# Performance work log

Hardware: AMD Instinct MI355X
Metric: run time of the kernel (lower is better)

The kernel has to match this reference:

```python
import jax, jax.numpy as jnp
import numpy as np

K = 9      # kernel size
DIL = 2    # dilation
PAD = 8    # padding -> same-size output


def unfold(x):
    """nd2col: (B,C,H,W) -> (B,C,K,K,H,W) patches with dilation/padding."""
    B, C, H, W = x.shape
    xp = jnp.pad(x, ((0, 0), (0, 0), (PAD, PAD), (PAD, PAD)))
    cols = jnp.stack(
        [xp[:, :, i * DIL:i * DIL + H, j * DIL:j * DIL + W]
         for i in range(K) for j in range(K)], axis=2)
    return cols.reshape(B, C, K, K, H, W)


def pac_kernel(f):
    """Gaussian adaptive kernel: exp(-0.5*||f_nbr - f_center||^2), shape (B,1,K,K,H,W)."""
    # center of the dilated patch (K//2, K//2) is the pixel itself
    d = unfold(f) - f[:, :, None, None, :, :]
    return jnp.exp(-0.5 * jnp.sum(d * d, axis=1, keepdims=True))


def pacconv(x, k, w, b):
    """Pixel-adaptive conv: unfold, modulate by guidance kernel, contract with weight."""
    cols = unfold(x)                                  # (B,Cin,K,K,H,W)
    out = jnp.einsum('bcklhw,ockl->bohw', cols * k, w)
    return out + b[None, :, None, None]


def setup_inputs() -> dict:
    key = jax.random.key(0)
    ks = jax.random.split(key, 6)
    B, C, H, W = 1, 32, 128, 128
    x = jax.random.normal(ks[0], (B, C, H, W), jnp.float32)
    f = jax.random.normal(ks[1], (B, C, H, W), jnp.float32)
    fan_in = C * K * K
    bound = float(1.0 / np.sqrt(fan_in))
    W1 = jax.random.uniform(ks[2], (32, C, K, K), jnp.float32, -bound, bound)
    b1 = jax.random.uniform(ks[3], (32,), jnp.float32, -bound, bound)
    W2 = jax.random.uniform(ks[4], (32, 32, K, K), jnp.float32, -bound, bound)
    b2 = jax.random.uniform(ks[5], (32,), jnp.float32, -bound, bound)
    return {"x": x, "f": f, "W1": W1, "b1": b1, "W2": W2, "b2": b2}


def reference(x, f, W1, b1, W2, b2):
    k = pac_kernel(f)  # same guidance for both layers -> identical kernel
    h = pacconv(x, k, W1, b1)
    return pacconv(h, k, W2, b2)
```

## Files before the change

### kernel.cpp

```cpp
#include <hip/hip_runtime.h>

#define HH 128
#define WW 128
#define NPIX 16384
#define NC 32
#define NO 32
#define KS 9
#define TAPS 81
#define DIL 2
#define PAD 8
#define SMAX 27.6310211159f
#define NW (NO * NC * TAPS)
#define CAP 262144

#define BUILD_MASK(P, M0, M1) do {                                          \
        M0 = 0ull; M1 = 0u;                                                 \
        _Pragma("unroll")                                                   \
        for (int i_ = 0; i_ < 7; ++i_) {                                    \
            unsigned v_ = mask2[i_ * NPIX + (P)];                           \
            unsigned m_ = (v_ & 31u) | (((v_ >> 8) & 15u) << 5);            \
            M0 |= (unsigned long long)m_ << (9 * i_);                       \
        }                                                                   \
        {                                                                   \
            unsigned v7_ = mask2[7 * NPIX + (P)];                           \
            unsigned v8_ = mask2[8 * NPIX + (P)];                           \
            unsigned m7_ = (v7_ & 31u) | (((v7_ >> 8) & 15u) << 5);         \
            unsigned m8_ = (v8_ & 31u) | (((v8_ >> 8) & 15u) << 5);         \
            M0 |= (unsigned long long)(m7_ & 1u) << 63;                     \
            M1 = (m7_ >> 1) | (m8_ << 8);                                   \
        }                                                                   \
    } while (0)

__global__ __launch_bounds__(256) void front2_kernel(
    const float* __restrict__ x, const float* __restrict__ f,
    const float* __restrict__ W1, const float* __restrict__ W2,
    const float* __restrict__ b1,
    float* __restrict__ hd, float* __restrict__ kbuf,
    unsigned short* __restrict__ mask2, float* __restrict__ Mm,
    float* __restrict__ W1t, float* __restrict__ W2t,
    float* __restrict__ outz)
{
    const int bid = blockIdx.x;
    const int tid = threadIdx.x;
    __shared__ float shbuf[2048];

    if (bid < 1152) {
        const int pixblk = bid & 63, iz = bid >> 6;
        const int i = iz >> 1, z = iz & 1;
        const int pix = pixblk * 256 + tid;
        const int hh = pix >> 7, ww = pix & (WW - 1);
        float fc[NC];
#pragma unroll
        for (int c = 0; c < NC; ++c) fc[c] = f[c * NPIX + pix];
        const int qh = hh + i * DIL - PAD;
        const bool vh = (unsigned)qh < HH;
        const int j0 = z * 5;
        unsigned pmask = 0;
#pragma unroll
        for (int jj = 0; jj < 5; ++jj) {
            int j = j0 + jj;
            if (j < KS) {
                int qw = ww + j * DIL - PAD;
                bool valid = vh & ((unsigned)qw < WW);
                int q = valid ? (qh * WW + qw) : pix;
                float s0 = 0.f, s1 = 0.f, s2 = 0.f, s3 = 0.f;
#pragma unroll
                for (int c4 = 0; c4 < 8; ++c4) {
                    float d0 = f[(4 * c4 + 0) * NPIX + q] - fc[4 * c4 + 0];
                    float d1 = f[(4 * c4 + 1) * NPIX + q] - fc[4 * c4 + 1];
                    float d2 = f[(4 * c4 + 2) * NPIX + q] - fc[4 * c4 + 2];
                    float d3 = f[(4 * c4 + 3) * NPIX + q] - fc[4 * c4 + 3];
                    s0 = fmaf(d0, d0, s0); s1 = fmaf(d1, d1, s1);
                    s2 = fmaf(d2, d2, s2); s3 = fmaf(d3, d3, s3);
                }
                float s = (s0 + s1) + (s2 + s3);
                bool live = valid && (s <= SMAX) && !(i == 4 && j == 4);
                if (live) {
                    pmask |= 1u << jj;
                    kbuf[(i * KS + j) * NPIX + pix] = __expf(-0.5f * s);
                }
            }
        }
        ((unsigned char*)mask2)[2 * (i * NPIX + pix) + z] = (unsigned char)pmask;
        return;
    }

    if (bid < 1664) {
        const int r = bid - 1152;
        const int o0 = (r >> 6) * 4;
        const int pix = (r & 63) * 256 + tid;
        if (tid < 128)
            shbuf[tid] = W1[((o0 + (tid >> 5)) * NC + (tid & 31)) * TAPS + 40];
        __syncthreads();
        float x0[NC];
#pragma unroll
        for (int c = 0; c < NC; ++c) x0[c] = x[c * NPIX + pix];
        float a0 = 0.f, a1 = 0.f, a2 = 0.f, a3 = 0.f;
#pragma unroll
        for (int c = 0; c < NC; ++c) {
            float xv = x0[c];
            a0 = fmaf(xv, shbuf[0 * NC + c], a0);
            a1 = fmaf(xv, shbuf[1 * NC + c], a1);
            a2 = fmaf(xv, shbuf[2 * NC + c], a2);
            a3 = fmaf(xv, shbuf[3 * NC + c], a3);
        }
        hd[(o0 + 0) * NPIX + pix] = a0 + b1[o0 + 0];
        hd[(o0 + 1) * NPIX + pix] = a1 + b1[o0 + 1];
        hd[(o0 + 2) * NPIX + pix] = a2 + b1[o0 + 2];
        hd[(o0 + 3) * NPIX + pix] = a3 + b1[o0 + 3];
        return;
    }

    if (bid < 1792) {
        float4 z4 = make_float4(0.f, 0.f, 0.f, 0.f);
        for (int t = (bid - 1664) * 256 + tid; t < (NO * NPIX) / 4;
             t += 128 * 256)
            ((float4*)outz)[t] = z4;
        return;
    }

    if (bid < 1873) {
        const int T = bid - 1792;
        float* w2c_l = shbuf;
        float* w1t_l = shbuf + 1024;
        for (int t = tid; t < 1024; t += 256) {
            w2c_l[t] = W2[t * TAPS + 40];
            w1t_l[t] = W1[t * TAPS + T];
        }
        __syncthreads();
        for (int idx = tid; idx < 1024; idx += 256) {
            int o = idx >> 5, cp = idx & 31;
            float acc = 0.f;
#pragma unroll
            for (int c = 0; c < NC; ++c)
                acc = fmaf(w2c_l[o * NC + c], w1t_l[c * NC + cp], acc);
            Mm[(T * NO + o) * NC + cp] = acc;
        }
        return;
    }

    for (int t = (bid - 1873) * 256 + tid; t < NW; t += 64 * 256) {
        int o = t / (NC * TAPS);
        int r = t - o * (NC * TAPS);
        int c = r / TAPS;
        int tap = r - c * TAPS;
        int d = (tap * NO + o) * NC + c;
        W1t[d] = W1[t];
        W2t[d] = W2[t];
    }
}

__global__ __launch_bounds__(256) void back2_kernel(
    const float* __restrict__ x, const float* __restrict__ hd,
    const float* __restrict__ kbuf, const unsigned short* __restrict__ mask2,
    const float* __restrict__ Mm, const float* __restrict__ W1t,
    const float* __restrict__ W2t, const float* __restrict__ W2,
    const float* __restrict__ b2, float* __restrict__ out)
{
    const int bid = blockIdx.x;
    const int tid = threadIdx.x;

    if (bid < 512) {
        __shared__ float wsm[4 * NC];
        const int o0 = (bid >> 6) * 4;
        const int pix = (bid & 63) * 256 + tid;
        if (tid < 128)
            wsm[tid] = W2[((o0 + (tid >> 5)) * NC + (tid & 31)) * TAPS + 40];
        __syncthreads();
        float h0[NC];
#pragma unroll
        for (int c = 0; c < NC; ++c) h0[c] = hd[c * NPIX + pix];
        float a0 = 0.f, a1 = 0.f, a2 = 0.f, a3 = 0.f;
#pragma unroll
        for (int c = 0; c < NC; ++c) {
            float hv = h0[c];
            a0 = fmaf(hv, wsm[0 * NC + c], a0);
            a1 = fmaf(hv, wsm[1 * NC + c], a1);
            a2 = fmaf(hv, wsm[2 * NC + c], a2);
            a3 = fmaf(hv, wsm[3 * NC + c], a3);
        }
        atomicAdd(&out[(o0 + 0) * NPIX + pix], a0 + b2[o0 + 0]);
        atomicAdd(&out[(o0 + 1) * NPIX + pix], a1 + b2[o0 + 1]);
        atomicAdd(&out[(o0 + 2) * NPIX + pix], a2 + b2[o0 + 2]);
        atomicAdd(&out[(o0 + 3) * NPIX + pix], a3 + b2[o0 + 3]);
        return;
    }

    __shared__ float u_lds[8][NC];
    const int hw = tid >> 5;
    const int lane = tid & 31;
    const int pbase = (bid - 512) * 32;

    for (int pp = hw; pp < 32; pp += 8) {
        const int p = pbase + pp;
        unsigned long long A0; unsigned A1;
        BUILD_MASK(p, A0, A1);
        while (A0 || A1) {
            int T;
            if (A0) { T = __builtin_ctzll(A0); A0 &= A0 - 1; }
            else    { T = 64 + __builtin_ctz(A1); A1 &= A1 - 1; }
            const int ii = T / KS, jj = T - KS * ii;
            const int q = p + (ii * DIL - PAD) * WW + (jj * DIL - PAD);
            const float kv = kbuf[T * NPIX + p];

            float w2r[NC], mr[NC];
            {
                const float4* w2p = (const float4*)(W2t + (T * NO + lane) * NC);
                const float4* mp  = (const float4*)(Mm  + (T * NO + lane) * NC);
#pragma unroll
                for (int c4 = 0; c4 < 8; ++c4) {
                    float4 w4 = w2p[c4], m4 = mp[c4];
                    w2r[4 * c4 + 0] = w4.x; w2r[4 * c4 + 1] = w4.y;
                    w2r[4 * c4 + 2] = w4.z; w2r[4 * c4 + 3] = w4.w;
                    mr[4 * c4 + 0] = m4.x; mr[4 * c4 + 1] = m4.y;
                    mr[4 * c4 + 2] = m4.z; mr[4 * c4 + 3] = m4.w;
                }
            }

            float dot = 0.f;
#pragma unroll
            for (int c = 0; c < NC; ++c) {
                dot = fmaf(w2r[c], hd[c * NPIX + q], dot);
                dot = fmaf(mr[c],  x[c * NPIX + q],  dot);
            }

            float dsum = 0.f;
            unsigned long long B0; unsigned B1;
            BUILD_MASK(q, B0, B1);
            while (B0 || B1) {
                int T2;
                if (B0) { T2 = __builtin_ctzll(B0); B0 &= B0 - 1; }
                else    { T2 = 64 + __builtin_ctz(B1); B1 &= B1 - 1; }
                const int i2 = T2 / KS, j2 = T2 - KS * i2;
                const int q2 = q + (i2 * DIL - PAD) * WW + (j2 * DIL - PAD);
                const float kv2 = kbuf[T2 * NPIX + q];
                const float4* w1p =
                    (const float4*)(W1t + (T2 * NO + lane) * NC);
                float u = 0.f;
#pragma unroll
                for (int c4 = 0; c4 < 8; ++c4) {
                    float4 w4 = w1p[c4];
                    u = fmaf(w4.x, x[(4 * c4 + 0) * NPIX + q2], u);
                    u = fmaf(w4.y, x[(4 * c4 + 1) * NPIX + q2], u);
                    u = fmaf(w4.z, x[(4 * c4 + 2) * NPIX + q2], u);
                    u = fmaf(w4.w, x[(4 * c4 + 3) * NPIX + q2], u);
                }
                u_lds[hw][lane] = u;
                float dd = 0.f;
#pragma unroll
                for (int c = 0; c < NC; ++c)
                    dd = fmaf(w2r[c], u_lds[hw][c], dd);
                dsum = fmaf(kv2, dd, dsum);
            }
            atomicAdd(&out[lane * NPIX + p], kv * (dot + dsum));
        }
    }
}

__global__ __launch_bounds__(64) void zero_cnt_kernel(unsigned* __restrict__ cnt)
{
    if (threadIdx.x == 0) *cnt = 0u;
}

__device__ __forceinline__ void sparse_body(
    const float* __restrict__ in, const float* __restrict__ Wt,
    const unsigned* __restrict__ cnt, const uint2* __restrict__ list,
    float* __restrict__ out, unsigned gid, unsigned stride)
{
    unsigned n = *cnt;
    if (n > CAP) n = CAP;
    const unsigned total = n * 32u;
    for (unsigned it = gid; it < total; it += stride) {
        unsigned e = it >> 5;
        int o = (int)(it & 31u);
        uint2 me = list[e];
        int pix = (int)(me.x & 16383u);
        int T = (int)(me.x >> 14);
        float kv = __uint_as_float(me.y);
        int ii = T / KS, jj = T - KS * ii;
        int q = pix + (ii * DIL - PAD) * WW + (jj * DIL - PAD);
        const float4* __restrict__ wp =
            (const float4*)(Wt + (T * NO + o) * NC);
        float t0 = 0.f, t1 = 0.f, t2 = 0.f, t3 = 0.f;
#pragma unroll
        for (int c4 = 0; c4 < 8; ++c4) {
            float4 w4 = wp[c4];
            t0 = fmaf(in[(4 * c4 + 0) * NPIX + q], w4.x, t0);
            t1 = fmaf(in[(4 * c4 + 1) * NPIX + q], w4.y, t1);
            t2 = fmaf(in[(4 * c4 + 2) * NPIX + q], w4.z, t2);
            t3 = fmaf(in[(4 * c4 + 3) * NPIX + q], w4.w, t3);
        }
        atomicAdd(&out[o * NPIX + pix], kv * ((t0 + t1) + (t2 + t3)));
    }
}

__global__ __launch_bounds__(256) void front_kernel(
    const float* __restrict__ x, const float* __restrict__ f,
    const float* __restrict__ W1, const float* __restrict__ W2,
    const float* __restrict__ b1,
    float* __restrict__ h, unsigned* __restrict__ cnt,
    uint2* __restrict__ list, float* __restrict__ W1t,
    float* __restrict__ W2t, float* __restrict__ outz)
{
    const int y = blockIdx.y;
    const int tid = threadIdx.x;

    if (y < 41) {
        const int pix = blockIdx.x * 256 + tid;
        const int hh = pix >> 7, ww = pix & (WW - 1);
        float fc[NC];
#pragma unroll
        for (int c = 0; c < NC; ++c) fc[c] = f[c * NPIX + pix];
#pragma unroll
        for (int u = 0; u < 2; ++u) {
            int T = 2 * y + u;
            if (T >= TAPS || T == 40) continue;
            int ii = T / KS, jj = T - KS * ii;
            int qh = hh + ii * DIL - PAD;
            int qw = ww + jj * DIL - PAD;
            bool valid = ((unsigned)qh < HH) & ((unsigned)qw < WW);
            int q = valid ? (qh * WW + qw) : pix;
            float s0 = 0.f, s1 = 0.f, s2 = 0.f, s3 = 0.f;
#pragma unroll
            for (int c4 = 0; c4 < 8; ++c4) {
                float d0 = f[(4 * c4 + 0) * NPIX + q] - fc[4 * c4 + 0];
                float d1 = f[(4 * c4 + 1) * NPIX + q] - fc[4 * c4 + 1];
                float d2 = f[(4 * c4 + 2) * NPIX + q] - fc[4 * c4 + 2];
                float d3 = f[(4 * c4 + 3) * NPIX + q] - fc[4 * c4 + 3];
                s0 = fmaf(d0, d0, s0); s1 = fmaf(d1, d1, s1);
                s2 = fmaf(d2, d2, s2); s3 = fmaf(d3, d3, s3);
            }
            float s = (s0 + s1) + (s2 + s3);
            if (valid && (s <= SMAX)) {
                unsigned idx = atomicAdd(cnt, 1u);
                if (idx < CAP)
                    list[idx] = make_uint2(
                        (unsigned)pix | ((unsigned)T << 14),
                        __float_as_uint(__expf(-0.5f * s)));
            }
        }
        return;
    }

    if (y < 49) {
        const int o0 = (y - 41) * 4;
        __shared__ float wsm[4 * NC];
        if (tid < 128) {
            int o = tid >> 5, c = tid & 31;
            wsm[tid] = W1[((o0 + o) * NC + c) * TAPS + 40];
        }
        __syncthreads();
        const int pix = blockIdx.x * 256 + tid;
        float x0[NC];
#pragma unroll
        for (int c = 0; c < NC; ++c) x0[c] = x[c * NPIX + pix];
        float a0 = 0.f, a1 = 0.f, a2 = 0.f, a3 = 0.f;
#pragma unroll
        for (int c = 0; c < NC; ++c) {
            float xv = x0[c];
            a0 = fmaf(xv, wsm[0 * NC + c], a0);
            a1 = fmaf(xv, wsm[1 * NC + c], a1);
            a2 = fmaf(xv, wsm[2 * NC + c], a2);
            a3 = fmaf(xv, wsm[3 * NC + c], a3);
        }
        h[(o0 + 0) * NPIX + pix] = a0 + b1[o0 + 0];
        h[(o0 + 1) * NPIX + pix] = a1 + b1[o0 + 1];
        h[(o0 + 2) * NPIX + pix] = a2 + b1[o0 + 2];
        h[(o0 + 3) * NPIX + pix] = a3 + b1[o0 + 3];
        return;
    }

    if (y == 49) {
        float4 z = make_float4(0.f, 0.f, 0.f, 0.f);
        for (int t = blockIdx.x * 256 + tid; t < (NO * NPIX) / 4; t += 64 * 256)
            ((float4*)outz)[t] = z;
        return;
    }

    for (int t = blockIdx.x * 256 + tid; t < NW; t += 64 * 256) {
        int o = t / (NC * TAPS);
        int r = t - o * (NC * TAPS);
        int c = r / TAPS;
        int tap = r - c * TAPS;
        int d = (tap * NO + o) * NC + c;
        W1t[d] = W1[t];
        W2t[d] = W2[t];
    }
}

__global__ __launch_bounds__(256) void sparse1_kernel(
    const float* __restrict__ x, const float* __restrict__ W1t,
    const unsigned* __restrict__ cnt, const uint2* __restrict__ list,
    float* __restrict__ h)
{
    sparse_body(x, W1t, cnt, list, h,
                blockIdx.x * 256 + threadIdx.x, gridDim.x * 256);
}

__global__ __launch_bounds__(256) void back_kernel(
    const float* __restrict__ h, const float* __restrict__ W2,
    const float* __restrict__ W2t, const float* __restrict__ b2,
    const unsigned* __restrict__ cnt, const uint2* __restrict__ list,
    float* __restrict__ out)
{
    const int y = blockIdx.y;
    const int tid = threadIdx.x;
    if (y < 8) {
        const int o0 = y * 4;
        __shared__ float wsm[4 * NC];
        if (tid < 128) {
            int o = tid >> 5, c = tid & 31;
            wsm[tid] = W2[((o0 + o) * NC + c) * TAPS + 40];
        }
        __syncthreads();
        const int pix = blockIdx.x * 256 + tid;
        float h0[NC];
#pragma unroll
        for (int c = 0; c < NC; ++c) h0[c] = h[c * NPIX + pix];
        float a0 = 0.f, a1 = 0.f, a2 = 0.f, a3 = 0.f;
#pragma unroll
        for (int c = 0; c < NC; ++c) {
            float hv = h0[c];
            a0 = fmaf(hv, wsm[0 * NC + c], a0);
            a1 = fmaf(hv, wsm[1 * NC + c], a1);
            a2 = fmaf(hv, wsm[2 * NC + c], a2);
            a3 = fmaf(hv, wsm[3 * NC + c], a3);
        }
        atomicAdd(&out[(o0 + 0) * NPIX + pix], a0 + b2[o0 + 0]);
        atomicAdd(&out[(o0 + 1) * NPIX + pix], a1 + b2[o0 + 1]);
        atomicAdd(&out[(o0 + 2) * NPIX + pix], a2 + b2[o0 + 2]);
        atomicAdd(&out[(o0 + 3) * NPIX + pix], a3 + b2[o0 + 3]);
        return;
    }
    sparse_body(h, W2t, cnt, list, out,
                blockIdx.x * 256 + tid, 64 * 256);
}

#define CHUNK 27
#define NCHUNK 3
#define KMIN 1e-6f
__global__ __launch_bounds__(256) void pac_layer_fuse(
    const float* __restrict__ in, const float* __restrict__ f,
    const float* __restrict__ Wt, const float* __restrict__ bias,
    float* __restrict__ out)
{
    __shared__ float wl[NC * CHUNK * 8];
    const int og = blockIdx.y;
    const int pix = blockIdx.x * 256 + threadIdx.x;
    const int h = pix >> 7, w = pix & (WW - 1);
    float acc[8];
#pragma unroll
    for (int i = 0; i < 8; ++i) acc[i] = 0.f;
    float fc[NC];
#pragma unroll
    for (int c = 0; c < NC; ++c) fc[c] = f[c * NPIX + pix];
    for (int ch = 0; ch < NCHUNK; ++ch) {
        __syncthreads();
        for (int idx = threadIdx.x; idx < NC * CHUNK * 8; idx += 256) {
            int t = idx % CHUNK;
            int c = (idx / CHUNK) % NC;
            int o = idx / (CHUNK * NC);
            wl[(c * CHUNK + t) * 8 + o] =
                Wt[(og * 8 + o) * (NC * TAPS) + c * TAPS + ch * CHUNK + t];
        }
        __syncthreads();
        for (int t = 0; t < CHUNK; ++t) {
            int tap = ch * CHUNK + t;
            int qh = h + (tap / KS) * DIL - PAD;
            int qw = w + (tap % KS) * DIL - PAD;
            bool valid = ((unsigned)qh < HH) & ((unsigned)qw < WW);
            int q = qh * WW + qw;
            float s = 0.f;
#pragma unroll
            for (int c = 0; c < NC; ++c) {
                float fn = valid ? f[c * NPIX + q] : 0.f;
                float d = fn - fc[c];
                s = fmaf(d, d, s);
            }
            float kv = __expf(-0.5f * s);
            if (__all((kv < KMIN) | (!valid))) continue;
            const float* wpp = &wl[t * 8];
#pragma unroll 8
            for (int c = 0; c < NC; ++c) {
                float v = valid ? in[c * NPIX + q] : 0.f;
                v *= kv;
#pragma unroll
                for (int o = 0; o < 8; ++o)
                    acc[o] = fmaf(v, wpp[c * CHUNK * 8 + o], acc[o]);
            }
        }
    }
#pragma unroll
    for (int o = 0; o < 8; ++o)
        out[(og * 8 + o) * NPIX + pix] = acc[o] + bias[og * 8 + o];
}

extern "C" void kernel_launch(void* const* d_in, const int* in_sizes, int n_in,
                              void* d_out, int out_size, void* d_ws, size_t ws_size,
                              hipStream_t stream)
{
    (void)in_sizes; (void)n_in; (void)out_size;
    const float* x  = (const float*)d_in[0];
    const float* f  = (const float*)d_in[1];
    const float* W1 = (const float*)d_in[2];
    const float* b1 = (const float*)d_in[3];
    const float* W2 = (const float*)d_in[4];
    const float* b2 = (const float*)d_in[5];
    float* out = (float*)d_out;

    float* ws = (float*)d_ws;
    float* hd   = ws;
    float* kbuf = hd + NO * NPIX;
    float* W1t  = kbuf + TAPS * NPIX;
    float* W2t  = W1t + NW;
    float* Mm   = W2t + NW;
    unsigned short* mask2 = (unsigned short*)(Mm + TAPS * NO * NC);
    const size_t need_main =
        (size_t)(NO * NPIX + TAPS * NPIX + 2 * NW + TAPS * NO * NC) * 4
        + (size_t)KS * NPIX * 2;
    float* hA   = ws;
    float* W1tA = ws + NO * NPIX;
    float* W2tA = W1tA + NW;
    unsigned* cnt = (unsigned*)(W2tA + NW);
    uint2* list = (uint2*)(cnt + 16);
    const size_t need_fb =
        (size_t)(NO * NPIX + 2 * NW + 16) * 4 + (size_t)CAP * 8;

    if (ws_size >= need_main) {
        front2_kernel<<<dim3(1937), 256, 0, stream>>>(
            x, f, W1, W2, b1, hd, kbuf, mask2, Mm, W1t, W2t, out);
        back2_kernel<<<dim3(1024), 256, 0, stream>>>(
            x, hd, kbuf, mask2, Mm, W1t, W2t, W2, b2, out);
    } else if (ws_size >= need_fb) {
        zero_cnt_kernel<<<dim3(1), 64, 0, stream>>>(cnt);
        front_kernel<<<dim3(64, 51), 256, 0, stream>>>(
            x, f, W1, W2, b1, hA, cnt, list, W1tA, W2tA, out);
        sparse1_kernel<<<dim3(128), 256, 0, stream>>>(x, W1tA, cnt, list, hA);
        back_kernel<<<dim3(64, 9), 256, 0, stream>>>(
            hA, W2, W2tA, b2, cnt, list, out);
    } else {
        float* hbuf = ws;
        pac_layer_fuse<<<dim3(64, 4), 256, 0, stream>>>(x, f, W1, b1, hbuf);
        pac_layer_fuse<<<dim3(64, 4), 256, 0, stream>>>(hbuf, f, W2, b2, out);
    }
}
```

Measured before the change: 120.3 us.

## Store tap masks per pixel contiguously and give each back-kernel warp one pixel

The front kernel now splits each kernel row into three groups of three taps instead of two groups of five. It writes the per-pixel mask bytes contiguously, 32 bytes per pixel. The back kernel builds the 81-bit tap mask with two 16-byte vector loads instead of nine strided short loads. Each half-warp group now handles a single pixel and the back grid grows from 1024 to 2560 blocks, which spreads the irregular sparse work across more blocks. The trade-offs are more front blocks, a larger mask buffer and more launch overhead.

```diff
diff --git a/kernel.cpp b/kernel.cpp
--- a/kernel.cpp
+++ b/kernel.cpp
@@ -13,22 +13,26 @@
 #define NW (NO * NC * TAPS)
 #define CAP 262144
 
-#define BUILD_MASK(P, M0, M1) do {                                          \
+#define BUILD_MASK32(P, M0, M1) do {                                        \
+        const uint4* mp_ = (const uint4*)(mask32 + (size_t)(P) * 32);       \
+        uint4 ma_ = mp_[0], mb_ = mp_[1];                                   \
+        unsigned w_[8] = { ma_.x, ma_.y, ma_.z, ma_.w,                      \
+                           mb_.x, mb_.y, mb_.z, mb_.w };                    \
         M0 = 0ull; M1 = 0u;                                                 \
+        unsigned m9_[9];                                                    \
         _Pragma("unroll")                                                   \
-        for (int i_ = 0; i_ < 7; ++i_) {                                    \
-            unsigned v_ = mask2[i_ * NPIX + (P)];                           \
-            unsigned m_ = (v_ & 31u) | (((v_ >> 8) & 15u) << 5);            \
-            M0 |= (unsigned long long)m_ << (9 * i_);                       \
+        for (int i_ = 0; i_ < 9; ++i_) {                                    \
+            int k0_ = 3 * i_, k1_ = 3 * i_ + 1, k2_ = 3 * i_ + 2;           \
+            unsigned b0_ = (w_[k0_ >> 2] >> ((k0_ & 3) * 8)) & 7u;          \
+            unsigned b1_ = (w_[k1_ >> 2] >> ((k1_ & 3) * 8)) & 7u;          \
+            unsigned b2_ = (w_[k2_ >> 2] >> ((k2_ & 3) * 8)) & 7u;          \
+            m9_[i_] = b0_ | (b1_ << 3) | (b2_ << 6);                        \
         }                                                                   \
-        {                                                                   \
-            unsigned v7_ = mask2[7 * NPIX + (P)];                           \
-            unsigned v8_ = mask2[8 * NPIX + (P)];                           \
-            unsigned m7_ = (v7_ & 31u) | (((v7_ >> 8) & 15u) << 5);         \
-            unsigned m8_ = (v8_ & 31u) | (((v8_ >> 8) & 15u) << 5);         \
-            M0 |= (unsigned long long)(m7_ & 1u) << 63;                     \
-            M1 = (m7_ >> 1) | (m8_ << 8);                                   \
-        }                                                                   \
+        _Pragma("unroll")                                                   \
+        for (int i_ = 0; i_ < 7; ++i_)                                      \
+            M0 |= (unsigned long long)m9_[i_] << (9 * i_);                  \
+        M0 |= (unsigned long long)(m9_[7] & 1u) << 63;                      \
+        M1 = (m9_[7] >> 1) | (m9_[8] << 8);                                 \
     } while (0)
 
 __global__ __launch_bounds__(256) void front2_kernel(
@@ -36,7 +40,7 @@
     const float* __restrict__ W1, const float* __restrict__ W2,
     const float* __restrict__ b1,
     float* __restrict__ hd, float* __restrict__ kbuf,
-    unsigned short* __restrict__ mask2, float* __restrict__ Mm,
+    unsigned char* __restrict__ mask32, float* __restrict__ Mm,
     float* __restrict__ W1t, float* __restrict__ W2t,
     float* __restrict__ outz)
 {
@@ -44,9 +48,9 @@
     const int tid = threadIdx.x;
     __shared__ float shbuf[2048];
 
-    if (bid < 1152) {
+    if (bid < 1728) {
         const int pixblk = bid & 63, iz = bid >> 6;
-        const int i = iz >> 1, z = iz & 1;
+        const int i = iz / 3, z = iz - 3 * i;
         const int pix = pixblk * 256 + tid;
         const int hh = pix >> 7, ww = pix & (WW - 1);
         float fc[NC];
@@ -54,39 +58,36 @@
         for (int c = 0; c < NC; ++c) fc[c] = f[c * NPIX + pix];
         const int qh = hh + i * DIL - PAD;
         const bool vh = (unsigned)qh < HH;
-        const int j0 = z * 5;
         unsigned pmask = 0;
 #pragma unroll
-        for (int jj = 0; jj < 5; ++jj) {
-            int j = j0 + jj;
-            if (j < KS) {
-                int qw = ww + j * DIL - PAD;
-                bool valid = vh & ((unsigned)qw < WW);
-                int q = valid ? (qh * WW + qw) : pix;
-                float s0 = 0.f, s1 = 0.f, s2 = 0.f, s3 = 0.f;
-#pragma unroll
-                for (int c4 = 0; c4 < 8; ++c4) {
-                    float d0 = f[(4 * c4 + 0) * NPIX + q] - fc[4 * c4 + 0];
-                    float d1 = f[(4 * c4 + 1) * NPIX + q] - fc[4 * c4 + 1];
-                    float d2 = f[(4 * c4 + 2) * NPIX + q] - fc[4 * c4 + 2];
-                    float d3 = f[(4 * c4 + 3) * NPIX + q] - fc[4 * c4 + 3];
-                    s0 = fmaf(d0, d0, s0); s1 = fmaf(d1, d1, s1);
-                    s2 = fmaf(d2, d2, s2); s3 = fmaf(d3, d3, s3);
-                }
-                float s = (s0 + s1) + (s2 + s3);
-                bool live = valid && (s <= SMAX) && !(i == 4 && j == 4);
-                if (live) {
-                    pmask |= 1u << jj;
-                    kbuf[(i * KS + j) * NPIX + pix] = __expf(-0.5f * s);
-                }
-            }
-        }
-        ((unsigned char*)mask2)[2 * (i * NPIX + pix) + z] = (unsigned char)pmask;
-        return;
-    }
-
-    if (bid < 1664) {
-        const int r = bid - 1152;
+        for (int jj = 0; jj < 3; ++jj) {
+            int j = 3 * z + jj;
+            int qw = ww + j * DIL - PAD;
+            bool valid = vh & ((unsigned)qw < WW);
+            int q = valid ? (qh * WW + qw) : pix;
+            float s0 = 0.f, s1 = 0.f, s2 = 0.f, s3 = 0.f;
+#pragma unroll
+            for (int c4 = 0; c4 < 8; ++c4) {
+                float d0 = f[(4 * c4 + 0) * NPIX + q] - fc[4 * c4 + 0];
+                float d1 = f[(4 * c4 + 1) * NPIX + q] - fc[4 * c4 + 1];
+                float d2 = f[(4 * c4 + 2) * NPIX + q] - fc[4 * c4 + 2];
+                float d3 = f[(4 * c4 + 3) * NPIX + q] - fc[4 * c4 + 3];
+                s0 = fmaf(d0, d0, s0); s1 = fmaf(d1, d1, s1);
+                s2 = fmaf(d2, d2, s2); s3 = fmaf(d3, d3, s3);
+            }
+            float s = (s0 + s1) + (s2 + s3);
+            bool live = valid && (s <= SMAX) && !(i == 4 && j == 4);
+            if (live) {
+                pmask |= 1u << jj;
+                kbuf[(i * KS + j) * NPIX + pix] = __expf(-0.5f * s);
+            }
+        }
+        mask32[(size_t)pix * 32 + iz] = (unsigned char)pmask;
+        return;
+    }
+
+    if (bid < 2240) {
+        const int r = bid - 1728;
         const int o0 = (r >> 6) * 4;
         const int pix = (r & 63) * 256 + tid;
         if (tid < 128)
@@ -111,16 +112,16 @@
         return;
     }
 
-    if (bid < 1792) {
+    if (bid < 2368) {
         float4 z4 = make_float4(0.f, 0.f, 0.f, 0.f);
-        for (int t = (bid - 1664) * 256 + tid; t < (NO * NPIX) / 4;
+        for (int t = (bid - 2240) * 256 + tid; t < (NO * NPIX) / 4;
              t += 128 * 256)
             ((float4*)outz)[t] = z4;
         return;
     }
 
-    if (bid < 1873) {
-        const int T = bid - 1792;
+    if (bid < 2449) {
+        const int T = bid - 2368;
         float* w2c_l = shbuf;
         float* w1t_l = shbuf + 1024;
         for (int t = tid; t < 1024; t += 256) {
@@ -139,7 +140,7 @@
         return;
     }
 
-    for (int t = (bid - 1873) * 256 + tid; t < NW; t += 64 * 256) {
+    for (int t = (bid - 2449) * 256 + tid; t < NW; t += 64 * 256) {
         int o = t / (NC * TAPS);
         int r = t - o * (NC * TAPS);
         int c = r / TAPS;
@@ -152,7 +153,7 @@
 
 __global__ __launch_bounds__(256) void back2_kernel(
     const float* __restrict__ x, const float* __restrict__ hd,
-    const float* __restrict__ kbuf, const unsigned short* __restrict__ mask2,
+    const float* __restrict__ kbuf, const unsigned char* __restrict__ mask32,
     const float* __restrict__ Mm, const float* __restrict__ W1t,
     const float* __restrict__ W2t, const float* __restrict__ W2,
     const float* __restrict__ b2, float* __restrict__ out)
@@ -189,71 +190,67 @@
     __shared__ float u_lds[8][NC];
     const int hw = tid >> 5;
     const int lane = tid & 31;
-    const int pbase = (bid - 512) * 32;
-
-    for (int pp = hw; pp < 32; pp += 8) {
-        const int p = pbase + pp;
-        unsigned long long A0; unsigned A1;
-        BUILD_MASK(p, A0, A1);
-        while (A0 || A1) {
-            int T;
-            if (A0) { T = __builtin_ctzll(A0); A0 &= A0 - 1; }
-            else    { T = 64 + __builtin_ctz(A1); A1 &= A1 - 1; }
-            const int ii = T / KS, jj = T - KS * ii;
-            const int q = p + (ii * DIL - PAD) * WW + (jj * DIL - PAD);
-            const float kv = kbuf[T * NPIX + p];
-
-            float w2r[NC], mr[NC];
-            {
-                const float4* w2p = (const float4*)(W2t + (T * NO + lane) * NC);
-                const float4* mp  = (const float4*)(Mm  + (T * NO + lane) * NC);
-#pragma unroll
-                for (int c4 = 0; c4 < 8; ++c4) {
-                    float4 w4 = w2p[c4], m4 = mp[c4];
-                    w2r[4 * c4 + 0] = w4.x; w2r[4 * c4 + 1] = w4.y;
-                    w2r[4 * c4 + 2] = w4.z; w2r[4 * c4 + 3] = w4.w;
-                    mr[4 * c4 + 0] = m4.x; mr[4 * c4 + 1] = m4.y;
-                    mr[4 * c4 + 2] = m4.z; mr[4 * c4 + 3] = m4.w;
-                }
-            }
-
-            float dot = 0.f;
-#pragma unroll
-            for (int c = 0; c < NC; ++c) {
-                dot = fmaf(w2r[c], hd[c * NPIX + q], dot);
-                dot = fmaf(mr[c],  x[c * NPIX + q],  dot);
-            }
-
-            float dsum = 0.f;
-            unsigned long long B0; unsigned B1;
-            BUILD_MASK(q, B0, B1);
-            while (B0 || B1) {
-                int T2;
-                if (B0) { T2 = __builtin_ctzll(B0); B0 &= B0 - 1; }
-                else    { T2 = 64 + __builtin_ctz(B1); B1 &= B1 - 1; }
-                const int i2 = T2 / KS, j2 = T2 - KS * i2;
-                const int q2 = q + (i2 * DIL - PAD) * WW + (j2 * DIL - PAD);
-                const float kv2 = kbuf[T2 * NPIX + q];
-                const float4* w1p =
-                    (const float4*)(W1t + (T2 * NO + lane) * NC);
-                float u = 0.f;
-#pragma unroll
-                for (int c4 = 0; c4 < 8; ++c4) {
-                    float4 w4 = w1p[c4];
-                    u = fmaf(w4.x, x[(4 * c4 + 0) * NPIX + q2], u);
-                    u = fmaf(w4.y, x[(4 * c4 + 1) * NPIX + q2], u);
-                    u = fmaf(w4.z, x[(4 * c4 + 2) * NPIX + q2], u);
-                    u = fmaf(w4.w, x[(4 * c4 + 3) * NPIX + q2], u);
-                }
-                u_lds[hw][lane] = u;
-                float dd = 0.f;
-#pragma unroll
-                for (int c = 0; c < NC; ++c)
-                    dd = fmaf(w2r[c], u_lds[hw][c], dd);
-                dsum = fmaf(kv2, dd, dsum);
-            }
-            atomicAdd(&out[lane * NPIX + p], kv * (dot + dsum));
-        }
+    const int p = (bid - 512) * 8 + hw;
+
+    unsigned long long A0; unsigned A1;
+    BUILD_MASK32(p, A0, A1);
+    while (A0 || A1) {
+        int T;
+        if (A0) { T = __builtin_ctzll(A0); A0 &= A0 - 1; }
+        else    { T = 64 + __builtin_ctz(A1); A1 &= A1 - 1; }
+        const int ii = T / KS, jj = T - KS * ii;
+        const int q = p + (ii * DIL - PAD) * WW + (jj * DIL - PAD);
+        const float kv = kbuf[T * NPIX + p];
+
+        float w2r[NC], mr[NC];
+        {
+            const float4* w2p = (const float4*)(W2t + (T * NO + lane) * NC);
+            const float4* mp  = (const float4*)(Mm  + (T * NO + lane) * NC);
+#pragma unroll
+            for (int c4 = 0; c4 < 8; ++c4) {
+                float4 w4 = w2p[c4], m4 = mp[c4];
+                w2r[4 * c4 + 0] = w4.x; w2r[4 * c4 + 1] = w4.y;
+                w2r[4 * c4 + 2] = w4.z; w2r[4 * c4 + 3] = w4.w;
+                mr[4 * c4 + 0] = m4.x; mr[4 * c4 + 1] = m4.y;
+                mr[4 * c4 + 2] = m4.z; mr[4 * c4 + 3] = m4.w;
+            }
+        }
+
+        float dot = 0.f;
+#pragma unroll
+        for (int c = 0; c < NC; ++c) {
+            dot = fmaf(w2r[c], hd[c * NPIX + q], dot);
+            dot = fmaf(mr[c],  x[c * NPIX + q],  dot);
+        }
+
+        float dsum = 0.f;
+        unsigned long long B0; unsigned B1;
+        BUILD_MASK32(q, B0, B1);
+        while (B0 || B1) {
+            int T2;
+            if (B0) { T2 = __builtin_ctzll(B0); B0 &= B0 - 1; }
+            else    { T2 = 64 + __builtin_ctz(B1); B1 &= B1 - 1; }
+            const int i2 = T2 / KS, j2 = T2 - KS * i2;
+            const int q2 = q + (i2 * DIL - PAD) * WW + (j2 * DIL - PAD);
+            const float kv2 = kbuf[T2 * NPIX + q];
+            const float4* w1p = (const float4*)(W1t + (T2 * NO + lane) * NC);
+            float u = 0.f;
+#pragma unroll
+            for (int c4 = 0; c4 < 8; ++c4) {
+                float4 w4 = w1p[c4];
+                u = fmaf(w4.x, x[(4 * c4 + 0) * NPIX + q2], u);
+                u = fmaf(w4.y, x[(4 * c4 + 1) * NPIX + q2], u);
+                u = fmaf(w4.z, x[(4 * c4 + 2) * NPIX + q2], u);
+                u = fmaf(w4.w, x[(4 * c4 + 3) * NPIX + q2], u);
+            }
+            u_lds[hw][lane] = u;
+            float dd = 0.f;
+#pragma unroll
+            for (int c = 0; c < NC; ++c)
+                dd = fmaf(w2r[c], u_lds[hw][c], dd);
+            dsum = fmaf(kv2, dd, dsum);
+        }
+        atomicAdd(&out[lane * NPIX + p], kv * (dot + dsum));
     }
 }
 
@@ -514,10 +511,10 @@
     float* W1t  = kbuf + TAPS * NPIX;
     float* W2t  = W1t + NW;
     float* Mm   = W2t + NW;
-    unsigned short* mask2 = (unsigned short*)(Mm + TAPS * NO * NC);
+    unsigned char* mask32 = (unsigned char*)(Mm + TAPS * NO * NC);
     const size_t need_main =
         (size_t)(NO * NPIX + TAPS * NPIX + 2 * NW + TAPS * NO * NC) * 4
-        + (size_t)KS * NPIX * 2;
+        + (size_t)NPIX * 32;
     float* hA   = ws;
     float* W1tA = ws + NO * NPIX;
     float* W2tA = W1tA + NW;
@@ -527,10 +524,10 @@
         (size_t)(NO * NPIX + 2 * NW + 16) * 4 + (size_t)CAP * 8;
 
     if (ws_size >= need_main) {
-        front2_kernel<<<dim3(1937), 256, 0, stream>>>(
-            x, f, W1, W2, b1, hd, kbuf, mask2, Mm, W1t, W2t, out);
-        back2_kernel<<<dim3(1024), 256, 0, stream>>>(
-            x, hd, kbuf, mask2, Mm, W1t, W2t, W2, b2, out);
+        front2_kernel<<<dim3(2513), 256, 0, stream>>>(
+            x, f, W1, W2, b1, hd, kbuf, mask32, Mm, W1t, W2t, out);
+        back2_kernel<<<dim3(2560), 256, 0, stream>>>(
+            x, hd, kbuf, mask32, Mm, W1t, W2t, W2, b2, out);
     } else if (ws_size >= need_fb) {
         zero_cnt_kernel<<<dim3(1), 64, 0, stream>>>(cnt);
         front_kernel<<<dim3(64, 51), 256, 0, stream>>>(
```

Measured after the change: 114.1 us. 1.05x faster.
